# Kernel tuning notes

Hardware: AMD Instinct MI355X
Metric: run time of the kernel (lower is better)

## Reference

```python
import jax, jax.numpy as jnp
import numpy as np

B, L, D, H, E, R, FF, K = 4, 1024, 1024, 16, 8, 64, 4096, 2
DH = D // H
EPS = 1e-5
SCALING = 2.0


def layer_norm(x, g, b):
    m = jnp.mean(x, axis=-1, keepdims=True)
    v = jnp.mean(jnp.square(x - m), axis=-1, keepdims=True)
    return (x - m) * jax.lax.rsqrt(v + EPS) * g + b


def setup_inputs() -> dict:
    key = jax.random.key(0)
    ks = jax.random.split(key, 16)
    s = 0.02
    return {
        "hidden_states": jax.random.normal(ks[0], (B, L, D), dtype=jnp.float32),
        "wq": jax.random.normal(ks[1], (D, D), dtype=jnp.float32) * s,
        "wk": jax.random.normal(ks[2], (D, D), dtype=jnp.float32) * s,
        "wv": jax.random.normal(ks[3], (D, D), dtype=jnp.float32) * s,
        "wo": jax.random.normal(ks[4], (D, D), dtype=jnp.float32) * s,
        "bq": jnp.zeros((D,), jnp.float32),
        "bk": jnp.zeros((D,), jnp.float32),
        "bv": jnp.zeros((D,), jnp.float32),
        "bo": jnp.zeros((D,), jnp.float32),
        "ln1_g": jnp.ones((D,), jnp.float32),
        "ln1_b": jnp.zeros((D,), jnp.float32),
        "w1": jax.random.normal(ks[5], (D, FF), dtype=jnp.float32) * s,
        "b1": jnp.zeros((FF,), jnp.float32),
        "w2": jax.random.normal(ks[6], (FF, D), dtype=jnp.float32) * s,
        "b2": jnp.zeros((D,), jnp.float32),
        "ln2_g": jnp.ones((D,), jnp.float32),
        "ln2_b": jnp.zeros((D,), jnp.float32),
        # adapter: dense1 D -> E*R, per-expert dense2 R -> D, gate D -> E
        "adp_w1": jax.random.normal(ks[7], (D, E * R), dtype=jnp.float32) * s,
        "adp_b1": jnp.zeros((E * R,), jnp.float32),
        "adp_w2": jax.random.normal(ks[8], (E, R, D), dtype=jnp.float32) * s,
        "adp_b2": jnp.zeros((E, D), jnp.float32),
        "gate_w": jax.random.normal(ks[9], (D, E), dtype=jnp.float32) * s,
        "gate_b": jnp.zeros((E,), jnp.float32),
    }


def reference(hidden_states, wq, wk, wv, wo, bq, bk, bv, bo, ln1_g, ln1_b,
              w1, b1, w2, b2, ln2_g, ln2_b,
              adp_w1, adp_b1, adp_w2, adp_b2, gate_w, gate_b):
    x = hidden_states
    # --- Roberta self-attention ---
    q = (x @ wq + bq).reshape(B, L, H, DH)
    k = (x @ wk + bk).reshape(B, L, H, DH)
    v = (x @ wv + bv).reshape(B, L, H, DH)
    scores = jnp.einsum("bqhd,bkhd->bhqk", q, k) / jnp.sqrt(jnp.float32(DH))
    probs = jax.nn.softmax(scores, axis=-1)
    ctx = jnp.einsum("bhqk,bkhd->bqhd", probs, v).reshape(B, L, D)
    attn_out = layer_norm(ctx @ wo + bo + x, ln1_g, ln1_b)

    # --- FFN (intermediate + output) ---
    inter = jax.nn.gelu(attn_out @ w1 + b1, approximate=False)
    layer_out = layer_norm(inter @ w2 + b2 + attn_out, ln2_g, ln2_b)

    # --- LoRA_MD_Adapter with NaiveGate (dense compute all experts, then combine) ---
    h = jax.nn.gelu(attn_out @ adp_w1 + adp_b1, approximate=False)  # [B,L,E*R]
    h = h.reshape(B, L, E, R)
    adp = jnp.einsum("bler,erd->bled", h, adp_w2) + adp_b2  # [B,L,E,D]
    logits = attn_out @ gate_w + gate_b  # [B,L,E]
    topv, topi = jax.lax.top_k(logits, K)  # [B,L,K]
    gate_score = jax.nn.softmax(topv, axis=-1)  # [B,L,K]
    # LoRA_MD combine: weight ALL per-expert outputs by top-k softmax scores
    # scattered to the selected experts, then sum over experts.
    picked = jnp.take_along_axis(adp, topi[..., None], axis=2)  # [B,L,K,D]
    adp_out = jnp.sum(picked * gate_score[..., None], axis=2) * SCALING  # [B,L,D]

    return layer_out + adp_out
```

## Files before the change

### kernel.cpp

```cpp
#include <hip/hip_runtime.h>
#include <cstddef>
#include <cstdint>

#define B_   4
#define L_   1024
#define D_   1024
#define H_   16
#define DH_  64
#define E_   8
#define R_   64
#define FF_  4096
#define NTOK (B_ * L_)

typedef __attribute__((ext_vector_type(8))) short bf16x8;
typedef __attribute__((ext_vector_type(4))) float f32x4;
typedef unsigned short us;

__device__ __forceinline__ float gelu_f(float x) {
  return 0.5f * x * (1.0f + erff(x * 0.7071067811865476f));
}

__device__ __forceinline__ us bf16_of(float f) {
  union { float f; uint32_t u; } x; x.f = f;
  uint32_t r = x.u + 0x7FFFu + ((x.u >> 16) & 1u);
  return (us)(r >> 16);
}
__device__ __forceinline__ float f32_of(us h) {
  union { uint32_t u; float f; } x; x.u = ((uint32_t)h) << 16;
  return x.f;
}
__device__ __forceinline__ void split_hl(float v, us& hi, us& lo) {
  hi = bf16_of(v);
  lo = bf16_of(v - f32_of(hi));
}

__device__ __forceinline__ void glds16(const void* g, const void* l) {
  __builtin_amdgcn_global_load_lds(
      (const __attribute__((address_space(1))) unsigned int*)g,
      (__attribute__((address_space(3))) unsigned int*)l, 16, 0, 0);
}

__global__ __launch_bounds__(256)
void fhi(const float* __restrict__ X, us* __restrict__ Hh, int n4) {
  int i = blockIdx.x * 256 + threadIdx.x;
  if (i >= n4) return;
  float4 v = ((const float4*)X)[i];
  ushort4 h = {bf16_of(v.x), bf16_of(v.y), bf16_of(v.z), bf16_of(v.w)};
  ((ushort4*)Hh)[i] = h;
}

__global__ __launch_bounds__(256)
void bconcat(const float* __restrict__ a, const float* __restrict__ b,
             const float* __restrict__ c, float* __restrict__ o) {
  int i = blockIdx.x * 256 + threadIdx.x;
  if (i >= 3072) return;
  o[i] = (i < 1024) ? a[i] : (i < 2048 ? b[i - 1024] : c[i - 2048]);
}

__global__ __launch_bounds__(256)
void wsplit_t(const float* __restrict__ W, us* __restrict__ Th,
              us* __restrict__ Tl, int K, int N) {
  __shared__ float tile[64][65];
  const int k0 = blockIdx.y * 64, n0 = blockIdx.x * 64;
  const int t = threadIdx.x;
  const int r = t >> 4, c4 = (t & 15) * 4;
  #pragma unroll
  for (int p = 0; p < 4; ++p) {
    const int k = r + p * 16;
    *(float4*)&tile[k][c4] = *(const float4*)&W[(size_t)(k0 + k) * N + n0 + c4];
  }
  __syncthreads();
  #pragma unroll
  for (int p = 0; p < 4; ++p) {
    const int n = r + p * 16;
    float v0 = tile[c4 + 0][n], v1 = tile[c4 + 1][n];
    float v2 = tile[c4 + 2][n], v3 = tile[c4 + 3][n];
    ushort4 h, l;
    split_hl(v0, h.x, l.x); split_hl(v1, h.y, l.y);
    split_hl(v2, h.z, l.z); split_hl(v3, h.w, l.w);
    const size_t o = (size_t)(n0 + n) * K + k0 + c4;
    *(ushort4*)&Th[o] = h;
    *(ushort4*)&Tl[o] = l;
  }
}

template<int EPI>
__global__ __launch_bounds__(256, 2)
void gemm128(const us* __restrict__ Ah,
             const us* __restrict__ Bh, const us* __restrict__ Bl,
             const float* __restrict__ bias, const float* __restrict__ ResF,
             float* __restrict__ Cf, int M, int N, int K) {
  __shared__ us sm3[3][3][4096];

  const int t = threadIdx.x;
  const int lane = t & 63, wid = t >> 6;
  const int wm = wid >> 1, wn = wid & 1;
  const int fr = lane & 15, fq = lane >> 4;
  const int rsw8 = (fq ^ ((fr >> 1) & 3)) * 8;

  const int nx = N >> 7;
  const int idl = blockIdx.x + blockIdx.y * nx;
  const int xcd = idl & 7, jj = idl >> 3;
  const int band = (M >> 7) >> 3;
  const int m0 = (xcd * band + (jj % band)) << 7;
  const int n0 = (jj / band) << 7;

  const int srow = t >> 2;
  const int gsub = t & 3;

  auto stage1 = [&](int buf, int kt, int idx) {
    const int stream = idx >> 1;
    const int half = idx & 1;
    const us* gp = (stream == 0) ? Ah : (stream == 1 ? Bh : Bl);
    const int row = half * 64 + srow;
    const int gchunk = gsub ^ ((row >> 1) & 3);
    const int rbase = ((stream == 0) ? m0 : n0) + row;
    const size_t g = (size_t)rbase * K + kt * 32 + gchunk * 8;
    glds16(gp + g, &sm3[buf][stream][row * 32 + gsub * 8]);
  };

  f32x4 acc[4][4];
  #pragma unroll
  for (int i = 0; i < 4; ++i)
    #pragma unroll
    for (int n = 0; n < 4; ++n) acc[i][n] = (f32x4){0.f, 0.f, 0.f, 0.f};

  #pragma unroll
  for (int idx = 0; idx < 6; ++idx) stage1(0, 0, idx);
  #pragma unroll
  for (int idx = 0; idx < 6; ++idx) stage1(1, 1, idx);

  const int nt = K >> 5;
  for (int g = 0; g < nt; ++g) {
    const int cb = g % 3;
    if (g < nt - 1) { asm volatile("s_waitcnt vmcnt(6)" ::: "memory"); }
    else            { asm volatile("s_waitcnt vmcnt(0)" ::: "memory"); }
    __builtin_amdgcn_sched_barrier(0);
    __builtin_amdgcn_s_barrier();
    __builtin_amdgcn_sched_barrier(0);

    const us* sA   = sm3[cb][0];
    const us* sBh_ = sm3[cb][1];
    const us* sBl_ = sm3[cb][2];

    bf16x8 bh[4], bl[4], av[4];
    #pragma unroll
    for (int n = 0; n < 4; ++n) {
      const int rb = (wn * 64 + n * 16 + fr) * 32 + rsw8;
      bh[n] = *(const bf16x8*)&sBh_[rb];
      bl[n] = *(const bf16x8*)&sBl_[rb];
    }
    #pragma unroll
    for (int i = 0; i < 4; ++i)
      av[i] = *(const bf16x8*)&sA[(wm * 64 + i * 16 + fr) * 32 + rsw8];

    const bool pf = (g + 2 < nt);
    const int nb = (g + 2) % 3;

    #pragma unroll
    for (int i = 0; i < 4; ++i) {
      if (pf && i < 3) { stage1(nb, g + 2, 2 * i); stage1(nb, g + 2, 2 * i + 1); }
      if (i == 0) {
        asm volatile("s_waitcnt lgkmcnt(0)" ::: "memory");
        __builtin_amdgcn_sched_barrier(0);
      }
      __builtin_amdgcn_s_setprio(1);
      #pragma unroll
      for (int n = 0; n < 4; ++n) {
        acc[i][n] = __builtin_amdgcn_mfma_f32_16x16x32_bf16(av[i], bh[n], acc[i][n], 0, 0, 0);
        acc[i][n] = __builtin_amdgcn_mfma_f32_16x16x32_bf16(av[i], bl[n], acc[i][n], 0, 0, 0);
      }
      __builtin_amdgcn_s_setprio(0);
    }
  }

  float bcol[4];
  #pragma unroll
  for (int n = 0; n < 4; ++n) bcol[n] = bias[n0 + wn * 64 + n * 16 + fr];

  #pragma unroll
  for (int i = 0; i < 4; ++i) {
    #pragma unroll
    for (int r = 0; r < 4; ++r) {
      const int row = m0 + wm * 64 + i * 16 + fq * 4 + r;
      const size_t ro = (size_t)row * N;
      #pragma unroll
      for (int n = 0; n < 4; ++n) {
        const int col = n0 + wn * 64 + n * 16 + fr;
        float v = acc[i][n][r] + bcol[n];
        if (EPI == 1) Cf[ro + col] = gelu_f(v);
        else          Cf[ro + col] = v + ResF[ro + col];
      }
    }
  }
}

template<int EPI>
__global__ __launch_bounds__(512, 2)
void gemm256(const us* __restrict__ Ah,
             const us* __restrict__ Bh, const us* __restrict__ Bl,
             const float* __restrict__ bias,
             float* __restrict__ Cf, us* __restrict__ Ch, us* __restrict__ Cl,
             us* __restrict__ Kh2, us* __restrict__ Kl2,
             us* __restrict__ Vh2, us* __restrict__ Vl2,
             int M, int N, int Kfull, int klen) {
  __shared__ us sm3[3][3][8192];

  const int t = threadIdx.x;
  const int lane = t & 63, wid = t >> 6;
  const int wm = wid >> 2, wn = wid & 3;
  const int fr = lane & 15, fq = lane >> 4;
  const int rsw8 = (fq ^ ((fr >> 1) & 3)) * 8;

  const int nx = N >> 8;
  const int idl = blockIdx.x + blockIdx.y * nx;
  const int xcd = idl & 7, jj = idl >> 3;
  const int band = (M >> 8) >> 3;
  const int m0 = (xcd * band + (jj % band)) << 8;
  const int n0 = (jj / band) << 8;
  const int koff = blockIdx.z * klen;

  const int srow = t >> 2;
  const int gchunk = (t & 3) ^ ((t >> 3) & 3);
  const int dso = srow * 32 + (t & 3) * 8;

  auto stage1 = [&](int buf, int kt, int idx) {
    const int stream = idx >> 1;
    const int half = idx & 1;
    const us* gp = (stream == 0) ? Ah : (stream == 1 ? Bh : Bl);
    const int rbase = ((stream == 0) ? m0 : n0) + half * 128 + srow;
    const size_t g = (size_t)rbase * Kfull + koff + kt * 32 + gchunk * 8;
    glds16(gp + g, &sm3[buf][stream][half * 4096 + dso]);
  };

  f32x4 acc[8][4];
  #pragma unroll
  for (int i = 0; i < 8; ++i)
    #pragma unroll
    for (int n = 0; n < 4; ++n) acc[i][n] = (f32x4){0.f, 0.f, 0.f, 0.f};

  #pragma unroll
  for (int idx = 0; idx < 6; ++idx) stage1(0, 0, idx);
  #pragma unroll
  for (int idx = 0; idx < 6; ++idx) stage1(1, 1, idx);

  const int nt = klen >> 5;
  bf16x8 bhf[4], blf[4];

#define PH_MFMA(qq)                                                              \
  {                                                                              \
    bf16x8 a0 = *(const bf16x8*)&sm3[cb][0][(wm * 128 + (2*qq) * 16 + fr) * 32 + rsw8];   \
    bf16x8 a1 = *(const bf16x8*)&sm3[cb][0][(wm * 128 + (2*qq+1) * 16 + fr) * 32 + rsw8]; \
    asm volatile("s_waitcnt lgkmcnt(0)" ::: "memory");                           \
    __builtin_amdgcn_sched_barrier(0);                                           \
    __builtin_amdgcn_s_setprio(1);                                               \
    _Pragma("unroll")                                                            \
    for (int n = 0; n < 4; ++n) {                                                \
      acc[2*qq][n]   = __builtin_amdgcn_mfma_f32_16x16x32_bf16(a0, bhf[n], acc[2*qq][n], 0,0,0);   \
      acc[2*qq][n]   = __builtin_amdgcn_mfma_f32_16x16x32_bf16(a0, blf[n], acc[2*qq][n], 0,0,0);   \
      acc[2*qq+1][n] = __builtin_amdgcn_mfma_f32_16x16x32_bf16(a1, bhf[n], acc[2*qq+1][n], 0,0,0); \
      acc[2*qq+1][n] = __builtin_amdgcn_mfma_f32_16x16x32_bf16(a1, blf[n], acc[2*qq+1][n], 0,0,0); \
    }                                                                            \
    __builtin_amdgcn_s_setprio(0);                                               \
  }

  for (int g = 0; g < nt; ++g) {
    const int cb = g % 3;
    if (g < nt - 1) { asm volatile("s_waitcnt vmcnt(6)" ::: "memory"); }
    else            { asm volatile("s_waitcnt vmcnt(0)" ::: "memory"); }
    __builtin_amdgcn_sched_barrier(0);
    __builtin_amdgcn_s_barrier();
    __builtin_amdgcn_sched_barrier(0);
    #pragma unroll
    for (int n = 0; n < 4; ++n) {
      const int rb = (wn * 64 + n * 16 + fr) * 32 + rsw8;
      bhf[n] = *(const bf16x8*)&sm3[cb][1][rb];
      blf[n] = *(const bf16x8*)&sm3[cb][2][rb];
    }
    const bool pf = (g + 2 < nt);
    const int nb = (g + 2) % 3;
    if (pf) { stage1(nb, g + 2, 0); stage1(nb, g + 2, 1); }
    PH_MFMA(0)
    if (pf) { stage1(nb, g + 2, 2); stage1(nb, g + 2, 3); }
    PH_MFMA(1)
    if (pf) { stage1(nb, g + 2, 4); stage1(nb, g + 2, 5); }
    PH_MFMA(2)
    PH_MFMA(3)
  }
#undef PH_MFMA

  if (EPI == 12) {
    float* pk = (blockIdx.z == 0) ? Cf :
                (blockIdx.z == 1) ? (float*)Kh2 :
                (blockIdx.z == 2) ? (float*)Kl2 : (float*)Vh2;
    #pragma unroll
    for (int i = 0; i < 8; ++i) {
      #pragma unroll
      for (int r = 0; r < 4; ++r) {
        const int row = m0 + wm * 128 + i * 16 + fq * 4 + r;
        const size_t ro = (size_t)row * N;
        #pragma unroll
        for (int n = 0; n < 4; ++n) {
          const int col = n0 + wn * 64 + n * 16 + fr;
          pk[ro + col] = acc[i][n][r];
        }
      }
    }
    return;
  }

  float bcol[4];
  #pragma unroll
  for (int n = 0; n < 4; ++n) bcol[n] = bias[n0 + wn * 64 + n * 16 + fr];

  if (EPI == 11) {
    #pragma unroll
    for (int i = 0; i < 8; ++i) {
      #pragma unroll
      for (int r = 0; r < 4; ++r) {
        const int row = m0 + wm * 128 + i * 16 + fq * 4 + r;
        const size_t ro = (size_t)row * N;
        #pragma unroll
        for (int n = 0; n < 4; ++n) {
          const int col = n0 + wn * 64 + n * 16 + fr;
          Ch[ro + col] = bf16_of(gelu_f(acc[i][n][r] + bcol[n]));
        }
      }
    }
    return;
  }

  {
    const int sel = n0 >> 10;
    if (sel < 2) {
      us* dh = (sel == 0) ? Ch : Kh2;
      us* dl = Cl;
      #pragma unroll
      for (int i = 0; i < 8; ++i) {
        #pragma unroll
        for (int r = 0; r < 4; ++r) {
          const int row = m0 + wm * 128 + i * 16 + fq * 4 + r;
          const size_t ro = (size_t)row * 1024;
          #pragma unroll
          for (int n = 0; n < 4; ++n) {
            const int c10 = (n0 & 1023) + wn * 64 + n * 16 + fr;
            float v = acc[i][n][r] + bcol[n];
            if (sel == 0) {
              us h, l; split_hl(v, h, l);
              dh[ro + c10] = h; dl[ro + c10] = l;
            } else {
              dh[ro + c10] = bf16_of(v);
            }
          }
        }
      }
    } else {
      #pragma unroll
      for (int i = 0; i < 8; ++i) {
        #pragma unroll
        for (int n = 0; n < 4; ++n) {
          const int c10 = (n0 & 1023) + wn * 64 + n * 16 + fr;
          const int hh2 = c10 >> 6, dh = c10 & 63;
          const int row0 = m0 + wm * 128 + i * 16 + fq * 4;
          const int bb = row0 >> 10, ltok = row0 & 1023;
          ushort4 h4, l4;
          float v0 = acc[i][n][0] + bcol[n];
          float v1 = acc[i][n][1] + bcol[n];
          float v2 = acc[i][n][2] + bcol[n];
          float v3 = acc[i][n][3] + bcol[n];
          split_hl(v0, h4.x, l4.x); split_hl(v1, h4.y, l4.y);
          split_hl(v2, h4.z, l4.z); split_hl(v3, h4.w, l4.w);
          const size_t off = ((size_t)(bb * 16 + hh2) * 64 + dh) * L_ + ltok;
          *(ushort4*)&Vh2[off] = h4;
          *(ushort4*)&Vl2[off] = l4;
        }
      }
    }
  }
}

__global__ __launch_bounds__(256, 4)
void attn_mfma(const us* __restrict__ Qh, const us* __restrict__ Ql,
               const us* __restrict__ Kh,
               const us* __restrict__ Vth, const us* __restrict__ Vtl,
               us* __restrict__ Oh) {
  const int raw = blockIdx.x + blockIdx.y * 16;
  const int hh = (raw & 7) + 8 * ((raw >> 3) >> 4);
  const int qq = (raw >> 3) & 15;
  const int b = hh >> 4, h = hh & 15;

  const int t = threadIdx.x;
  const int w = t >> 6, lane = t & 63;
  const int fr = lane & 15, g = lane >> 4;

  __shared__ __align__(16) unsigned char smem[33792];
  us* sK  = (us*)(smem);
  us* sVh = (us*)(smem + 8192);
  us* sVl = (us*)(smem + 16384);
  us* sP  = (us*)(smem + 24576);
  float* fb = (float*)smem;

  const size_t base = ((size_t)b * L_) * D_ + (size_t)h * DH_;
  const int tok0 = b * L_ + qq * 64 + w * 16;
  bf16x8 qfh[2], qfl[2];
  #pragma unroll
  for (int ks = 0; ks < 2; ++ks) {
    const size_t qo = (size_t)(tok0 + fr) * D_ + h * 64 + ks * 32 + g * 8;
    qfh[ks] = *(const bf16x8*)&Qh[qo];
    qfl[ks] = *(const bf16x8*)&Ql[qo];
  }

  const float Cc = 0.18033688011112042f;
  float m = -INFINITY, l = 0.0f;
  f32x4 ctx[4];
  #pragma unroll
  for (int i = 0; i < 4; ++i) ctx[i] = (f32x4){0.f, 0.f, 0.f, 0.f};
  const int rswk = (g ^ ((fr >> 1) & 3)) * 8;

  for (int kt = 0; kt < 16; ++kt) {
    const int k0 = kt * 64;
    __syncthreads();
    #pragma unroll
    for (int p = 0; p < 2; ++p) {
      const int ci = w * 128 + p * 64 + lane;
      const int db = ci * 8;
      {
        const int ks = ci >> 8, rem = ci & 255, key = rem >> 2, sub = rem & 3;
        const int subp = sub ^ ((key >> 1) & 3);
        glds16(Kh + base + (size_t)(k0 + key) * D_ + ks * 32 + subp * 8, sK + db);
      }
      {
        const int d = ci >> 3, c = ci & 7;
        const size_t src = (size_t)(hh * 64 + d) * L_ + k0 + ((c ^ (d & 7)) * 8);
        glds16(Vth + src, sVh + db);
        glds16(Vtl + src, sVl + db);
      }
    }
    __syncthreads();

    f32x4 accS[4];
    #pragma unroll
    for (int i = 0; i < 4; ++i) accS[i] = (f32x4){0.f, 0.f, 0.f, 0.f};
    #pragma unroll
    for (int ks = 0; ks < 2; ++ks) {
      #pragma unroll
      for (int i = 0; i < 4; ++i) {
        const int ra = (ks * 64 + i * 16 + fr) * 32 + rswk;
        bf16x8 a = *(const bf16x8*)&sK[ra];
        accS[i] = __builtin_amdgcn_mfma_f32_16x16x32_bf16(a, qfh[ks], accS[i], 0, 0, 0);
        accS[i] = __builtin_amdgcn_mfma_f32_16x16x32_bf16(a, qfl[ks], accS[i], 0, 0, 0);
      }
    }

    float p4[4][4];
    float mloc = -INFINITY;
    #pragma unroll
    for (int i = 0; i < 4; ++i)
      #pragma unroll
      for (int r = 0; r < 4; ++r) {
        p4[i][r] = accS[i][r] * Cc;
        mloc = fmaxf(mloc, p4[i][r]);
      }
    mloc = fmaxf(mloc, __shfl_xor(mloc, 16));
    mloc = fmaxf(mloc, __shfl_xor(mloc, 32));
    const float mnew = fmaxf(m, mloc);
    const float alpha = exp2f(m - mnew);
    float lt = 0.f;
    #pragma unroll
    for (int i = 0; i < 4; ++i)
      #pragma unroll
      for (int r = 0; r < 4; ++r) {
        p4[i][r] = exp2f(p4[i][r] - mnew);
        lt += p4[i][r];
      }
    lt += __shfl_xor(lt, 16);
    lt += __shfl_xor(lt, 32);
    l = l * alpha + lt;
    m = mnew;
    #pragma unroll
    for (int i = 0; i < 4; ++i) {
      ctx[i][0] *= alpha; ctx[i][1] *= alpha;
      ctx[i][2] *= alpha; ctx[i][3] *= alpha;
    }

    #pragma unroll
    for (int i = 0; i < 4; ++i) {
      us h0 = bf16_of(p4[i][0]), h1 = bf16_of(p4[i][1]);
      us h2 = bf16_of(p4[i][2]), h3 = bf16_of(p4[i][3]);
      uint2 hv = {(uint32_t)h0 | ((uint32_t)h1 << 16),
                  (uint32_t)h2 | ((uint32_t)h3 << 16)};
      *(uint2*)&sP[(w * 16 + fr) * 72 + i * 16 + g * 4] = hv;
    }

    #pragma unroll
    for (int ks = 0; ks < 2; ++ks) {
      const int pb = (w * 16 + fr) * 72 + ks * 32 + g * 8;
      bf16x8 pa = *(const bf16x8*)&sP[pb];
      #pragma unroll
      for (int i = 0; i < 4; ++i) {
        const int d = i * 16 + fr;
        const int pc = (ks * 4 + g) ^ (d & 7);
        bf16x8 vh = *(const bf16x8*)&sVh[d * 64 + pc * 8];
        bf16x8 vl = *(const bf16x8*)&sVl[d * 64 + pc * 8];
        ctx[i] = __builtin_amdgcn_mfma_f32_16x16x32_bf16(vh, pa, ctx[i], 0, 0, 0);
        ctx[i] = __builtin_amdgcn_mfma_f32_16x16x32_bf16(vl, pa, ctx[i], 0, 0, 0);
      }
    }
  }

  const float invl = 1.0f / l;
  __syncthreads();
  #pragma unroll
  for (int i = 0; i < 4; ++i)
    #pragma unroll
    for (int r = 0; r < 4; ++r)
      fb[(i * 16 + g * 4 + r) * 64 + w * 16 + fr] = ctx[i][r] * invl;
  __syncthreads();

  {
    const int q = t >> 2, dg = t & 3;
    const size_t ob = (size_t)(b * L_ + qq * 64 + q) * D_ + h * 64;
    #pragma unroll
    for (int u = 0; u < 4; ++u) {
      const int d0 = dg * 16 + u * 4;
      ushort4 h4 = {bf16_of(fb[(d0 + 0) * 64 + q]),
                    bf16_of(fb[(d0 + 1) * 64 + q]),
                    bf16_of(fb[(d0 + 2) * 64 + q]),
                    bf16_of(fb[(d0 + 3) * 64 + q])};
      *(ushort4*)&Oh[ob + d0] = h4;
    }
  }
}

template<int MODE>
__global__ __launch_bounds__(256)
void layernorm_k(const float* __restrict__ X, const float* __restrict__ g,
                 const float* __restrict__ b, float* __restrict__ Yf,
                 us* __restrict__ Yh, us* __restrict__ Yl) {
  const int row = blockIdx.x;
  const int t = threadIdx.x;
  const float* x = X + (size_t)row * D_;

  float4 v = *(const float4*)&x[t * 4];
  float s  = v.x + v.y + v.z + v.w;
  float ss = v.x * v.x + v.y * v.y + v.z * v.z + v.w * v.w;

  #pragma unroll
  for (int off = 1; off < 64; off <<= 1) {
    s  += __shfl_xor(s, off);
    ss += __shfl_xor(ss, off);
  }
  __shared__ float red[4][2];
  const int wid = t >> 6;
  if ((t & 63) == 0) { red[wid][0] = s; red[wid][1] = ss; }
  __syncthreads();
  s  = red[0][0] + red[1][0] + red[2][0] + red[3][0];
  ss = red[0][1] + red[1][1] + red[2][1] + red[3][1];

  const float mean = s * (1.0f / D_);
  const float var  = ss * (1.0f / D_) - mean * mean;
  const float inv  = rsqrtf(var + 1e-5f);

  float4 gv = *(const float4*)&g[t * 4];
  float4 bv = *(const float4*)&b[t * 4];
  float4 o;
  o.x = (v.x - mean) * inv * gv.x + bv.x;
  o.y = (v.y - mean) * inv * gv.y + bv.y;
  o.z = (v.z - mean) * inv * gv.z + bv.z;
  o.w = (v.w - mean) * inv * gv.w + bv.w;
  if (MODE == 0) {
    *(float4*)&Yf[(size_t)row * D_ + t * 4] = o;
  } else {
    ushort4 h, l;
    split_hl(o.x, h.x, l.x); split_hl(o.y, h.y, l.y);
    split_hl(o.z, h.z, l.z); split_hl(o.w, h.w, l.w);
    *(ushort4*)&Yh[(size_t)row * D_ + t * 4] = h;
    *(ushort4*)&Yl[(size_t)row * D_ + t * 4] = l;
  }
}

__global__ __launch_bounds__(256)
void lnred4(const float* __restrict__ P0, const float* __restrict__ P1,
            const float* __restrict__ P2, const float* __restrict__ P3,
            const float* __restrict__ b2,
            const us* __restrict__ Rh, const us* __restrict__ Rl,
            const float* __restrict__ g, const float* __restrict__ be,
            float* __restrict__ Y) {
  const int row = blockIdx.x;
  const int t = threadIdx.x;
  const size_t o = (size_t)row * D_ + t * 4;

  float4 v0 = *(const float4*)&P0[o];
  float4 v1 = *(const float4*)&P1[o];
  float4 v2 = *(const float4*)&P2[o];
  float4 v3 = *(const float4*)&P3[o];
  float4 bb = *(const float4*)&b2[t * 4];
  ushort4 rh = *(const ushort4*)&Rh[o];
  ushort4 rl = *(const ushort4*)&Rl[o];
  float4 v;
  v.x = v0.x + v1.x + v2.x + v3.x + bb.x + f32_of(rh.x) + f32_of(rl.x);
  v.y = v0.y + v1.y + v2.y + v3.y + bb.y + f32_of(rh.y) + f32_of(rl.y);
  v.z = v0.z + v1.z + v2.z + v3.z + bb.z + f32_of(rh.z) + f32_of(rl.z);
  v.w = v0.w + v1.w + v2.w + v3.w + bb.w + f32_of(rh.w) + f32_of(rl.w);

  float s  = v.x + v.y + v.z + v.w;
  float ss = v.x * v.x + v.y * v.y + v.z * v.z + v.w * v.w;
  #pragma unroll
  for (int off = 1; off < 64; off <<= 1) {
    s  += __shfl_xor(s, off);
    ss += __shfl_xor(ss, off);
  }
  __shared__ float red[4][2];
  const int wid = t >> 6;
  if ((t & 63) == 0) { red[wid][0] = s; red[wid][1] = ss; }
  __syncthreads();
  s  = red[0][0] + red[1][0] + red[2][0] + red[3][0];
  ss = red[0][1] + red[1][1] + red[2][1] + red[3][1];

  const float mean = s * (1.0f / D_);
  const float var  = ss * (1.0f / D_) - mean * mean;
  const float inv  = rsqrtf(var + 1e-5f);

  float4 gv = *(const float4*)&g[t * 4];
  float4 bv = *(const float4*)&be[t * 4];
  float4 y;
  y.x = (v.x - mean) * inv * gv.x + bv.x;
  y.y = (v.y - mean) * inv * gv.y + bv.y;
  y.z = (v.z - mean) * inv * gv.z + bv.z;
  y.w = (v.w - mean) * inv * gv.w + bv.w;
  *(float4*)&Y[o] = y;
}

__global__ __launch_bounds__(256)
void adapter_combine_hl(const us* __restrict__ Xh, const us* __restrict__ Xl,
                        const float* __restrict__ Hall,
                        const float* __restrict__ Lout,
                        const us* __restrict__ W2b,
                        const float* __restrict__ B2,
                        const float* __restrict__ GW,
                        const float* __restrict__ GB,
                        float* __restrict__ Out) {
  const int tok = blockIdx.x;
  const int t = threadIdx.x;

  __shared__ float xs[D_];
  __shared__ float part[256];
  __shared__ float logit_s[E_];
  __shared__ float hs[2 * R_];
  __shared__ int   e_sh[2];
  __shared__ float g_sh[2];

  {
    ushort4 h = *(const ushort4*)&Xh[(size_t)tok * D_ + t * 4];
    ushort4 l = *(const ushort4*)&Xl[(size_t)tok * D_ + t * 4];
    xs[t * 4 + 0] = f32_of(h.x) + f32_of(l.x);
    xs[t * 4 + 1] = f32_of(h.y) + f32_of(l.y);
    xs[t * 4 + 2] = f32_of(h.z) + f32_of(l.z);
    xs[t * 4 + 3] = f32_of(h.w) + f32_of(l.w);
  }
  __syncthreads();

  {
    const int e = t & 7, seg = t >> 3;
    float p = 0.f;
    #pragma unroll 8
    for (int i = 0; i < 32; ++i) {
      const int d = seg * 32 + i;
      p = fmaf(xs[d], GW[d * E_ + e], p);
    }
    part[t] = p;
  }
  __syncthreads();
  if (t < E_) {
    float s = GB[t];
    for (int sg = 0; sg < 32; ++sg) s += part[sg * 8 + t];
    logit_s[t] = s;
  }
  __syncthreads();
  if (t == 0) {
    int e1 = 0; float v1 = logit_s[0];
    for (int i = 1; i < E_; ++i) if (logit_s[i] > v1) { v1 = logit_s[i]; e1 = i; }
    int e2 = -1; float v2 = -INFINITY;
    for (int i = 0; i < E_; ++i) if (i != e1 && logit_s[i] > v2) { v2 = logit_s[i]; e2 = i; }
    const float ee = expf(v2 - v1);
    const float den = 1.0f + ee;
    g_sh[0] = 1.0f / den; g_sh[1] = ee / den;
    e_sh[0] = e1; e_sh[1] = e2;
  }
  __syncthreads();
  const int e1 = e_sh[0], e2 = e_sh[1];
  const float g1 = g_sh[0], g2 = g_sh[1];

  if (t < 2 * R_) {
    const int ex = (t < R_) ? e1 : e2;
    const int r = t & (R_ - 1);
    hs[t] = Hall[(size_t)tok * (E_ * R_) + ex * R_ + r];
  }
  __syncthreads();

  const int d = t * 4;
  float4 b1v = *(const float4*)&B2[e1 * D_ + d];
  float4 b2v = *(const float4*)&B2[e2 * D_ + d];
  float4 acc;
  acc.x = g1 * b1v.x + g2 * b2v.x;
  acc.y = g1 * b1v.y + g2 * b2v.y;
  acc.z = g1 * b1v.z + g2 * b2v.z;
  acc.w = g1 * b1v.w + g2 * b2v.w;

  #pragma unroll 8
  for (int r = 0; r < R_; ++r) {
    const float f = g1 * hs[r];
    ushort4 w = *(const ushort4*)&W2b[((size_t)e1 * R_ + r) * D_ + d];
    acc.x = fmaf(f, f32_of(w.x), acc.x); acc.y = fmaf(f, f32_of(w.y), acc.y);
    acc.z = fmaf(f, f32_of(w.z), acc.z); acc.w = fmaf(f, f32_of(w.w), acc.w);
  }
  #pragma unroll 8
  for (int r = 0; r < R_; ++r) {
    const float f = g2 * hs[R_ + r];
    ushort4 w = *(const ushort4*)&W2b[((size_t)e2 * R_ + r) * D_ + d];
    acc.x = fmaf(f, f32_of(w.x), acc.x); acc.y = fmaf(f, f32_of(w.y), acc.y);
    acc.z = fmaf(f, f32_of(w.z), acc.z); acc.w = fmaf(f, f32_of(w.w), acc.w);
  }

  float4 lo = *(const float4*)&Lout[(size_t)tok * D_ + d];
  float4 o = {lo.x + 2.0f * acc.x, lo.y + 2.0f * acc.y,
              lo.z + 2.0f * acc.z, lo.w + 2.0f * acc.w};
  *(float4*)&Out[(size_t)tok * D_ + d] = o;
}

extern "C" void kernel_launch(void* const* d_in, const int* in_sizes, int n_in,
                              void* d_out, int out_size, void* d_ws, size_t ws_size,
                              hipStream_t stream) {
  const float* x     = (const float*)d_in[0];
  const float* wq    = (const float*)d_in[1];
  const float* wk    = (const float*)d_in[2];
  const float* wv    = (const float*)d_in[3];
  const float* wo    = (const float*)d_in[4];
  const float* bq    = (const float*)d_in[5];
  const float* bk    = (const float*)d_in[6];
  const float* bv    = (const float*)d_in[7];
  const float* bo    = (const float*)d_in[8];
  const float* ln1g  = (const float*)d_in[9];
  const float* ln1b  = (const float*)d_in[10];
  const float* w1    = (const float*)d_in[11];
  const float* b1    = (const float*)d_in[12];
  const float* w2    = (const float*)d_in[13];
  const float* b2    = (const float*)d_in[14];
  const float* ln2g  = (const float*)d_in[15];
  const float* ln2b  = (const float*)d_in[16];
  const float* aw1   = (const float*)d_in[17];
  const float* ab1   = (const float*)d_in[18];
  const float* aw2   = (const float*)d_in[19];
  const float* ab2   = (const float*)d_in[20];
  const float* gw    = (const float*)d_in[21];
  const float* gb    = (const float*)d_in[22];
  float* out = (float*)d_out;

  char* base = (char*)d_ws;
  const size_t MB = 1ull << 20;

  us* qkvTh = (us*)(base + 0 * MB);  us* qkvTl = (us*)(base + 6 * MB);
  us* woTh  = (us*)(base + 12 * MB); us* woTl  = (us*)(base + 14 * MB);
  us* w1Th  = (us*)(base + 16 * MB); us* w1Tl  = (us*)(base + 24 * MB);
  us* w2Th  = (us*)(base + 32 * MB); us* w2Tl  = (us*)(base + 40 * MB);
  us* a1Th  = (us*)(base + 48 * MB); us* a1Tl  = (us*)(base + 49 * MB);
  us* w2b   = (us*)(base + 50 * MB);
  float* bqkv = (float*)(base + 51 * MB);
  us* xh   = (us*)(base + 52 * MB);
  us* ctxh = (us*)(base + 52 * MB);
  us* qbh  = (us*)(base + 68 * MB);  us* qbl  = (us*)(base + 76 * MB);
  us* kbh  = (us*)(base + 84 * MB);
  us* vth  = (us*)(base + 100 * MB); us* vtl  = (us*)(base + 108 * MB);
  float* ATTNPRE = (float*)(base + 68 * MB);
  us* aoh  = (us*)(base + 84 * MB);  us* aol  = (us*)(base + 92 * MB);
  us* inth = (us*)(base + 116 * MB);
  float* P0 = (float*)(base + 52 * MB);
  float* P1 = (float*)(base + 68 * MB);
  float* P2 = (float*)(base + 100 * MB);
  float* P3 = (float*)(base + 148 * MB);
  float* LOUT = P0;
  float* HALL = (float*)(base + 68 * MB);

  const dim3 blk(256);
  const us* nu = nullptr;
  const float* nf = nullptr;

  fhi<<<dim3(NTOK * D_ / 1024), blk, 0, stream>>>(x, xh, NTOK * D_ / 4);
  wsplit_t<<<dim3(16, 16), blk, 0, stream>>>(wq, qkvTh, qkvTl, D_, D_);
  wsplit_t<<<dim3(16, 16), blk, 0, stream>>>(wk, qkvTh + 1024 * 1024, qkvTl + 1024 * 1024, D_, D_);
  wsplit_t<<<dim3(16, 16), blk, 0, stream>>>(wv, qkvTh + 2048 * 1024, qkvTl + 2048 * 1024, D_, D_);
  wsplit_t<<<dim3(16, 16), blk, 0, stream>>>(wo, woTh, woTl, D_, D_);
  wsplit_t<<<dim3(64, 16), blk, 0, stream>>>(w1, w1Th, w1Tl, D_, FF_);
  wsplit_t<<<dim3(16, 64), blk, 0, stream>>>(w2, w2Th, w2Tl, FF_, D_);
  wsplit_t<<<dim3(8, 16),  blk, 0, stream>>>(aw1, a1Th, a1Tl, D_, E_ * R_);
  fhi<<<dim3(E_ * R_ * D_ / 1024), blk, 0, stream>>>(aw2, w2b, E_ * R_ * D_ / 4);
  bconcat<<<dim3(12), blk, 0, stream>>>(bq, bk, bv, bqkv);

  gemm256<10><<<dim3(12, 16), dim3(512), 0, stream>>>(
      xh, qkvTh, qkvTl, bqkv, nullptr, qbh, qbl, kbh, nullptr, vth, vtl,
      NTOK, 3072, D_, D_);
  attn_mfma<<<dim3(16, 64), blk, 0, stream>>>(qbh, qbl, kbh, vth, vtl, ctxh);
  gemm128<2><<<dim3(8, 32), blk, 0, stream>>>(ctxh, woTh, woTl, bo, x,
                                              ATTNPRE, NTOK, D_, D_);
  layernorm_k<1><<<dim3(NTOK), blk, 0, stream>>>(ATTNPRE, ln1g, ln1b, nullptr, aoh, aol);
  gemm256<11><<<dim3(16, 16), dim3(512), 0, stream>>>(
      aoh, w1Th, w1Tl, b1, nullptr, inth, nullptr, nullptr, nullptr, nullptr, nullptr,
      NTOK, FF_, D_, D_);
  gemm256<12><<<dim3(4, 16, 4), dim3(512), 0, stream>>>(
      inth, w2Th, w2Tl, nf, P0, nullptr, nullptr, (us*)P1, (us*)P2, (us*)P3, nullptr,
      NTOK, D_, FF_, 1024);
  lnred4<<<dim3(NTOK), blk, 0, stream>>>(P0, P1, P2, P3, b2, aoh, aol, ln2g, ln2b, LOUT);
  gemm128<1><<<dim3(4, 32), blk, 0, stream>>>(aoh, a1Th, a1Tl, ab1, nf,
                                              HALL, NTOK, E_ * R_, D_);
  adapter_combine_hl<<<dim3(NTOK), blk, 0, stream>>>(aoh, aol, HALL, LOUT, w2b, ab2, gw, gb, out);
}
```

Baseline: 571.4 us.

## Recast adapter expert combine as a gated MFMA GEMM with folded biases

The per-token scalar adapter combine, which gathered two experts' weights per token, is replaced by a gate kernel. That kernel writes a gate-scaled hidden vector of 512 values plus 8 gate weights, padded to K=576, as bf16. A gemm128 epilogue then multiplies it by a flattened [aw2; ab2] weight split into hi/lo bf16 parts and adds 2x the result to the layer output. This moves the expert projection onto MFMA with weight reuse across tokens, at the cost of computing all 8 experts densely (zeros for unselected ones). It also rounds the scaled activations to a single bf16 and adds an extra weight-prep transpose.

```diff
diff --git a/kernel.cpp b/kernel.cpp
--- a/kernel.cpp
+++ b/kernel.cpp
@@ -11,6 +11,7 @@
 #define R_   64
 #define FF_  4096
 #define NTOK (B_ * L_)
+#define KADP 576
 
 typedef __attribute__((ext_vector_type(8))) short bf16x8;
 typedef __attribute__((ext_vector_type(4))) float f32x4;
@@ -55,6 +56,19 @@
   int i = blockIdx.x * 256 + threadIdx.x;
   if (i >= 3072) return;
   o[i] = (i < 1024) ? a[i] : (i < 2048 ? b[i - 1024] : c[i - 2048]);
+}
+
+__global__ __launch_bounds__(256)
+void bflat_fill(const float* __restrict__ aw2, const float* __restrict__ ab2,
+                float* __restrict__ Bf) {
+  int i = blockIdx.x * 256 + threadIdx.x;
+  if (i >= KADP * 1024 / 4) return;
+  const int row = i >> 8;
+  float4 v;
+  if (row < 512)      v = ((const float4*)aw2)[i];
+  else if (row < 520) v = ((const float4*)ab2)[i - 512 * 256];
+  else                v = (float4){0.f, 0.f, 0.f, 0.f};
+  ((float4*)Bf)[i] = v;
 }
 
 __global__ __launch_bounds__(256)
@@ -175,8 +189,10 @@
   }
 
   float bcol[4];
-  #pragma unroll
-  for (int n = 0; n < 4; ++n) bcol[n] = bias[n0 + wn * 64 + n * 16 + fr];
+  if (EPI != 3) {
+    #pragma unroll
+    for (int n = 0; n < 4; ++n) bcol[n] = bias[n0 + wn * 64 + n * 16 + fr];
+  }
 
   #pragma unroll
   for (int i = 0; i < 4; ++i) {
@@ -187,9 +203,13 @@
       #pragma unroll
       for (int n = 0; n < 4; ++n) {
         const int col = n0 + wn * 64 + n * 16 + fr;
-        float v = acc[i][n][r] + bcol[n];
-        if (EPI == 1) Cf[ro + col] = gelu_f(v);
-        else          Cf[ro + col] = v + ResF[ro + col];
+        if (EPI == 1) {
+          Cf[ro + col] = gelu_f(acc[i][n][r] + bcol[n]);
+        } else if (EPI == 2) {
+          Cf[ro + col] = acc[i][n][r] + bcol[n] + ResF[ro + col];
+        } else {
+          Cf[ro + col] = ResF[ro + col] + 2.0f * acc[i][n][r];
+        }
       }
     }
   }
@@ -532,11 +552,10 @@
   }
 }
 
-template<int MODE>
 __global__ __launch_bounds__(256)
-void layernorm_k(const float* __restrict__ X, const float* __restrict__ g,
-                 const float* __restrict__ b, float* __restrict__ Yf,
-                 us* __restrict__ Yh, us* __restrict__ Yl) {
+void layernorm_hl(const float* __restrict__ X, const float* __restrict__ g,
+                  const float* __restrict__ b,
+                  us* __restrict__ Yh, us* __restrict__ Yl) {
   const int row = blockIdx.x;
   const int t = threadIdx.x;
   const float* x = X + (size_t)row * D_;
@@ -568,15 +587,11 @@
   o.y = (v.y - mean) * inv * gv.y + bv.y;
   o.z = (v.z - mean) * inv * gv.z + bv.z;
   o.w = (v.w - mean) * inv * gv.w + bv.w;
-  if (MODE == 0) {
-    *(float4*)&Yf[(size_t)row * D_ + t * 4] = o;
-  } else {
-    ushort4 h, l;
-    split_hl(o.x, h.x, l.x); split_hl(o.y, h.y, l.y);
-    split_hl(o.z, h.z, l.z); split_hl(o.w, h.w, l.w);
-    *(ushort4*)&Yh[(size_t)row * D_ + t * 4] = h;
-    *(ushort4*)&Yl[(size_t)row * D_ + t * 4] = l;
-  }
+  ushort4 h, l;
+  split_hl(o.x, h.x, l.x); split_hl(o.y, h.y, l.y);
+  split_hl(o.z, h.z, l.z); split_hl(o.w, h.w, l.w);
+  *(ushort4*)&Yh[(size_t)row * D_ + t * 4] = h;
+  *(ushort4*)&Yl[(size_t)row * D_ + t * 4] = l;
 }
 
 __global__ __launch_bounds__(256)
@@ -632,23 +647,17 @@
 }
 
 __global__ __launch_bounds__(256)
-void adapter_combine_hl(const us* __restrict__ Xh, const us* __restrict__ Xl,
-                        const float* __restrict__ Hall,
-                        const float* __restrict__ Lout,
-                        const us* __restrict__ W2b,
-                        const float* __restrict__ B2,
-                        const float* __restrict__ GW,
-                        const float* __restrict__ GB,
-                        float* __restrict__ Out) {
+void gate_scale(const us* __restrict__ Xh, const us* __restrict__ Xl,
+                const float* __restrict__ Hall,
+                const float* __restrict__ GW, const float* __restrict__ GB,
+                us* __restrict__ Aout) {
   const int tok = blockIdx.x;
   const int t = threadIdx.x;
 
   __shared__ float xs[D_];
   __shared__ float part[256];
   __shared__ float logit_s[E_];
-  __shared__ float hs[2 * R_];
-  __shared__ int   e_sh[2];
-  __shared__ float g_sh[2];
+  __shared__ float g_sh[E_];
 
   {
     ushort4 h = *(const ushort4*)&Xh[(size_t)tok * D_ + t * 4];
@@ -684,48 +693,22 @@
     for (int i = 0; i < E_; ++i) if (i != e1 && logit_s[i] > v2) { v2 = logit_s[i]; e2 = i; }
     const float ee = expf(v2 - v1);
     const float den = 1.0f + ee;
-    g_sh[0] = 1.0f / den; g_sh[1] = ee / den;
-    e_sh[0] = e1; e_sh[1] = e2;
+    #pragma unroll
+    for (int i = 0; i < E_; ++i) g_sh[i] = 0.f;
+    g_sh[e1] = 1.0f / den;
+    g_sh[e2] = ee / den;
   }
   __syncthreads();
-  const int e1 = e_sh[0], e2 = e_sh[1];
-  const float g1 = g_sh[0], g2 = g_sh[1];
-
-  if (t < 2 * R_) {
-    const int ex = (t < R_) ? e1 : e2;
-    const int r = t & (R_ - 1);
-    hs[t] = Hall[(size_t)tok * (E_ * R_) + ex * R_ + r];
-  }
-  __syncthreads();
-
-  const int d = t * 4;
-  float4 b1v = *(const float4*)&B2[e1 * D_ + d];
-  float4 b2v = *(const float4*)&B2[e2 * D_ + d];
-  float4 acc;
-  acc.x = g1 * b1v.x + g2 * b2v.x;
-  acc.y = g1 * b1v.y + g2 * b2v.y;
-  acc.z = g1 * b1v.z + g2 * b2v.z;
-  acc.w = g1 * b1v.w + g2 * b2v.w;
-
-  #pragma unroll 8
-  for (int r = 0; r < R_; ++r) {
-    const float f = g1 * hs[r];
-    ushort4 w = *(const ushort4*)&W2b[((size_t)e1 * R_ + r) * D_ + d];
-    acc.x = fmaf(f, f32_of(w.x), acc.x); acc.y = fmaf(f, f32_of(w.y), acc.y);
-    acc.z = fmaf(f, f32_of(w.z), acc.z); acc.w = fmaf(f, f32_of(w.w), acc.w);
-  }
-  #pragma unroll 8
-  for (int r = 0; r < R_; ++r) {
-    const float f = g2 * hs[R_ + r];
-    ushort4 w = *(const ushort4*)&W2b[((size_t)e2 * R_ + r) * D_ + d];
-    acc.x = fmaf(f, f32_of(w.x), acc.x); acc.y = fmaf(f, f32_of(w.y), acc.y);
-    acc.z = fmaf(f, f32_of(w.z), acc.z); acc.w = fmaf(f, f32_of(w.w), acc.w);
-  }
-
-  float4 lo = *(const float4*)&Lout[(size_t)tok * D_ + d];
-  float4 o = {lo.x + 2.0f * acc.x, lo.y + 2.0f * acc.y,
-              lo.z + 2.0f * acc.z, lo.w + 2.0f * acc.w};
-  *(float4*)&Out[(size_t)tok * D_ + d] = o;
+
+  us* arow = Aout + (size_t)tok * KADP;
+  #pragma unroll
+  for (int k = t; k < 512; k += 256) {
+    const float gv = g_sh[k >> 6];
+    arow[k] = bf16_of(gv * Hall[(size_t)tok * 512 + k]);
+  }
+  if (t < 64) {
+    arow[512 + t] = (t < 8) ? bf16_of(g_sh[t]) : (us)0;
+  }
 }
 
 extern "C" void kernel_launch(void* const* d_in, const int* in_sizes, int n_in,
@@ -764,8 +747,6 @@
   us* w1Th  = (us*)(base + 16 * MB); us* w1Tl  = (us*)(base + 24 * MB);
   us* w2Th  = (us*)(base + 32 * MB); us* w2Tl  = (us*)(base + 40 * MB);
   us* a1Th  = (us*)(base + 48 * MB); us* a1Tl  = (us*)(base + 49 * MB);
-  us* w2b   = (us*)(base + 50 * MB);
-  float* bqkv = (float*)(base + 51 * MB);
   us* xh   = (us*)(base + 52 * MB);
   us* ctxh = (us*)(base + 52 * MB);
   us* qbh  = (us*)(base + 68 * MB);  us* qbl  = (us*)(base + 76 * MB);
@@ -780,9 +761,13 @@
   float* P3 = (float*)(base + 148 * MB);
   float* LOUT = P0;
   float* HALL = (float*)(base + 68 * MB);
+  us* Aarg   = (us*)(base + 76 * MB);
+  us* b2Th   = (us*)(base + 165 * MB);
+  us* b2Tl   = (us*)(base + 167 * MB);
+  float* Bflat = (float*)(base + 169 * MB);
+  float* bqkv  = (float*)(base + 172 * MB);
 
   const dim3 blk(256);
-  const us* nu = nullptr;
   const float* nf = nullptr;
 
   fhi<<<dim3(NTOK * D_ / 1024), blk, 0, stream>>>(x, xh, NTOK * D_ / 4);
@@ -793,7 +778,8 @@
   wsplit_t<<<dim3(64, 16), blk, 0, stream>>>(w1, w1Th, w1Tl, D_, FF_);
   wsplit_t<<<dim3(16, 64), blk, 0, stream>>>(w2, w2Th, w2Tl, FF_, D_);
   wsplit_t<<<dim3(8, 16),  blk, 0, stream>>>(aw1, a1Th, a1Tl, D_, E_ * R_);
-  fhi<<<dim3(E_ * R_ * D_ / 1024), blk, 0, stream>>>(aw2, w2b, E_ * R_ * D_ / 4);
+  bflat_fill<<<dim3(KADP * 1024 / 1024), blk, 0, stream>>>(aw2, ab2, Bflat);
+  wsplit_t<<<dim3(16, KADP / 64), blk, 0, stream>>>(Bflat, b2Th, b2Tl, KADP, D_);
   bconcat<<<dim3(12), blk, 0, stream>>>(bq, bk, bv, bqkv);
 
   gemm256<10><<<dim3(12, 16), dim3(512), 0, stream>>>(
@@ -802,7 +788,7 @@
   attn_mfma<<<dim3(16, 64), blk, 0, stream>>>(qbh, qbl, kbh, vth, vtl, ctxh);
   gemm128<2><<<dim3(8, 32), blk, 0, stream>>>(ctxh, woTh, woTl, bo, x,
                                               ATTNPRE, NTOK, D_, D_);
-  layernorm_k<1><<<dim3(NTOK), blk, 0, stream>>>(ATTNPRE, ln1g, ln1b, nullptr, aoh, aol);
+  layernorm_hl<<<dim3(NTOK), blk, 0, stream>>>(ATTNPRE, ln1g, ln1b, aoh, aol);
   gemm256<11><<<dim3(16, 16), dim3(512), 0, stream>>>(
       aoh, w1Th, w1Tl, b1, nullptr, inth, nullptr, nullptr, nullptr, nullptr, nullptr,
       NTOK, FF_, D_, D_);
@@ -812,5 +798,7 @@
   lnred4<<<dim3(NTOK), blk, 0, stream>>>(P0, P1, P2, P3, b2, aoh, aol, ln2g, ln2b, LOUT);
   gemm128<1><<<dim3(4, 32), blk, 0, stream>>>(aoh, a1Th, a1Tl, ab1, nf,
                                               HALL, NTOK, E_ * R_, D_);
-  adapter_combine_hl<<<dim3(NTOK), blk, 0, stream>>>(aoh, aol, HALL, LOUT, w2b, ab2, gw, gb, out);
-}
+  gate_scale<<<dim3(NTOK), blk, 0, stream>>>(aoh, aol, HALL, gw, gb, Aarg);
+  gemm128<3><<<dim3(8, 32), blk, 0, stream>>>(Aarg, b2Th, b2Tl, nf, LOUT,
+                                              out, NTOK, D_, KADP);
+}
```

Result: faster. 536.2 us (-6.2%).
